# Kernel optimization log

Measured on AMD Instinct MI355X. Metric: run time of the kernel, lower is better.

Reference implementation:

```python
import jax, jax.numpy as jnp
import numpy as np

DIM = 512
MAXP = 100
N_SAMPLED = MAXP - 2  # partitions 0 (whole) and 1 (singletons) handled analytically
KMAX = 6              # sampled partitions have 2..6 parts


def _make_part_masks(dim, n_sampled, kmax, seed=0):
    rng = np.random.default_rng(seed)
    masks = np.zeros((n_sampled, kmax, dim), dtype=bool)
    for p in range(n_sampled):
        n_parts = rng.integers(2, kmax + 1)
        assign = rng.integers(0, n_parts, size=dim)
        for k in range(n_parts):
            masks[p, k] = assign == k
    return masks


def setup_inputs() -> dict:
    key = jax.random.key(0)
    ks = jax.random.split(key, 10)
    B, S, D = 8, 4096, DIM
    x = jax.random.normal(ks[0], (B, S, D), dtype=jnp.float32)
    entropy_scales = jnp.ones((D,), dtype=jnp.float32)
    integration_weights = jnp.ones((MAXP,), dtype=jnp.float32)
    W1 = jax.random.normal(ks[1], (32, 1), dtype=jnp.float32) * 0.5
    b1 = jax.random.normal(ks[2], (32,), dtype=jnp.float32) * 0.1
    W2 = jax.random.normal(ks[3], (16, 32), dtype=jnp.float32) * 0.2
    b2 = jax.random.normal(ks[4], (16,), dtype=jnp.float32) * 0.1
    W3 = jax.random.normal(ks[5], (1, 16), dtype=jnp.float32) * 0.3
    b3 = jax.random.normal(ks[6], (1,), dtype=jnp.float32) * 0.1
    part_masks = jnp.asarray(_make_part_masks(D, N_SAMPLED, KMAX))  # [P,K,D] bool
    return {"x": x, "entropy_scales": entropy_scales,
            "integration_weights": integration_weights,
            "W1": W1, "b1": b1, "W2": W2, "b2": b2, "W3": W3, "b3": b3,
            "part_masks": part_masks}


def _phi(x, entropy_scales, integration_weights, W1, b1, W2, b2, W3, b3, part_masks):
    B, S, D = x.shape
    # ---- full-flatten entropy (per batch), H(softmax(x.reshape(B,-1))) ----
    lp = jax.nn.log_softmax(x.reshape(B, -1), axis=-1)
    H_full = -jnp.sum(jnp.exp(lp) * lp, axis=-1)                     # [B]
    h_full_scaled = H_full * entropy_scales.mean()                   # [B]
    h_whole = H_full.mean()                                          # partition idx 0

    # ---- singleton partition (idx 1): softmax over seq per (b,d) ----
    lps = jax.nn.log_softmax(x, axis=1)                              # [B,S,D]
    H_sd = -jnp.sum(jnp.exp(lps) * lps, axis=1)                      # [B,D]
    h_single = H_sd.mean(axis=0).sum()

    # ---- sampled partitions via masks: per part, softmax over (seq x part dims) ----
    xmax_d = x.max(axis=1)                                           # [B,D]
    ex = jnp.exp(x - xmax_d[:, None, :])                             # [B,S,D]
    e_d = ex.sum(axis=1)                                             # [B,D] sum exp(x - xmax_d)
    t_d = (ex * x).sum(axis=1)                                       # [B,D] sum exp(.)*x
    valid = part_masks.any(axis=-1)                                  # [P,K]
    neg = jnp.finfo(x.dtype).min
    gmax = jnp.max(jnp.where(part_masks[None], xmax_d[:, None, None, :], neg), axis=-1)  # [B,P,K]
    gmax = jnp.where(valid[None], gmax, 0.0)
    shift = jnp.exp(xmax_d[:, None, None, :] - gmax[..., None])      # [B,P,K,D] <= 1
    mf = part_masks.astype(x.dtype)
    Z = jnp.einsum('pkd,bd,bpkd->bpk', mf, e_d, shift)               # group partition fn
    T = jnp.einsum('pkd,bd,bpkd->bpk', mf, t_d, shift)
    Zs = jnp.where(valid[None], Z, 1.0)
    H_pk = gmax + jnp.log(Zs) - T / Zs                               # group entropy [B,P,K]
    H_pk = jnp.where(valid[None], H_pk, 0.0)
    h_sampled = H_pk.mean(axis=0).sum(axis=-1)                       # [P] sum of part entropies

    h_parts = jnp.concatenate([jnp.stack([h_whole, h_single]), h_sampled])   # [100]
    weighted = h_parts * jax.nn.sigmoid(integration_weights[: h_parts.shape[0]])
    min_part = weighted.min()

    raw_phi = h_full_scaled.mean() - min_part
    z = jnp.clip(raw_phi / 10.0, 0.0, 1.0)[None]                     # [1]
    h = jax.nn.relu(z @ W1.T + b1)
    h = jax.nn.relu(h @ W2.T + b2)
    conf = jax.nn.sigmoid(h @ W3.T + b3).squeeze(-1)                 # scalar
    return conf


def reference(x, entropy_scales, integration_weights, W1, b1, W2, b2, W3, b3, part_masks):
    return _phi(x, entropy_scales, integration_weights, W1, b1, W2, b2, W3, b3, part_masks)
```

## Files before the change

kernel.cpp:

```cpp
#include <hip/hip_runtime.h>
#include <math.h>

constexpr int Bv = 8;
constexpr int Sv = 4096;
constexpr int Dv = 512;
constexpr int NCv = 64;
constexpr int SCv = Sv / NCv;
constexpr int Pv = 98;
constexpr int Kv = 6;
constexpr int MAXPv = 100;
constexpr int GPv = 14;
constexpr int PPGv = 7;

typedef float v4f __attribute__((ext_vector_type(4)));

constexpr size_t OFF_MPART = 0;
constexpr size_t OFF_ZPART = OFF_MPART + (size_t)Bv * NCv * Dv;
constexpr size_t OFF_TPART = OFF_ZPART + (size_t)Bv * NCv * Dv;
constexpr size_t OFF_HFULL = OFF_TPART + (size_t)Bv * NCv * Dv;
constexpr size_t OFF_HSD   = OFF_HFULL + Bv;
constexpr size_t OFF_HBP   = OFF_HSD + Bv;

__device__ __forceinline__ float warpSum(float v) {
    for (int o = 32; o > 0; o >>= 1) v += __shfl_xor(v, o);
    return v;
}
__device__ __forceinline__ float warpMax(float v) {
    for (int o = 32; o > 0; o >>= 1) v = fmaxf(v, __shfl_xor(v, o));
    return v;
}
__device__ __forceinline__ float blockSum512(float v, float* red) {
    float s = warpSum(v);
    int lane = threadIdx.x & 63, w = threadIdx.x >> 6;
    __syncthreads();
    if (lane == 0) red[w] = s;
    __syncthreads();
    return red[0] + red[1] + red[2] + red[3] + red[4] + red[5] + red[6] + red[7];
}
__device__ __forceinline__ float blockMax512(float v, float* red) {
    float s = warpMax(v);
    int lane = threadIdx.x & 63, w = threadIdx.x >> 6;
    __syncthreads();
    if (lane == 0) red[w] = s;
    __syncthreads();
    float m = red[0];
    for (int i = 1; i < 8; i++) m = fmaxf(m, red[i]);
    return m;
}

#define UPD(v, m, z, t)                                        \
    {                                                          \
        float vv = (v);                                        \
        if (vv > m) {                                          \
            float r = __expf(m - vv);                          \
            z = z * r + 1.0f;                                  \
            t = t * r + vv;                                    \
            m = vv;                                            \
        } else {                                               \
            float e_ = __expf(vv - m);                         \
            z += e_;                                           \
            t += e_ * vv;                                      \
        }                                                      \
    }

__device__ __forceinline__ void mergeStats(float& m, float& z, float& t,
                                           float mb, float zb, float tb) {
    float nm = fmaxf(m, mb);
    float ra = __expf(m - nm);
    float rb = __expf(mb - nm);
    z = z * ra + zb * rb;
    t = t * ra + tb * rb;
    m = nm;
}

__device__ __forceinline__ float sigmoidf(float v) { return 1.0f / (1.0f + __expf(-v)); }

__global__ __launch_bounds__(512) void k1_partial(const float* __restrict__ x,
                                                  float* __restrict__ ws) {
    int c = blockIdx.x;
    int b = blockIdx.y;
    int tid = threadIdx.x;
    int dg = tid & 127;
    int sl = tid >> 7;

    const v4f* xv = (const v4f*)x;
    float m0 = -INFINITY, m1 = -INFINITY, m2 = -INFINITY, m3 = -INFINITY;
    float z0 = 0.f, z1 = 0.f, z2 = 0.f, z3 = 0.f;
    float t0 = 0.f, t1 = 0.f, t2 = 0.f, t3 = 0.f;

    int sbase = c * SCv + sl;
#pragma unroll 4
    for (int i = 0; i < SCv / 4; i++) {
        int s = sbase + 4 * i;
        v4f v = __builtin_nontemporal_load(&xv[((size_t)b * Sv + s) * 128 + dg]);
        UPD(v.x, m0, z0, t0);
        UPD(v.y, m1, z1, t1);
        UPD(v.z, m2, z2, t2);
        UPD(v.w, m3, z3, t3);
    }

    __shared__ float smm[1024], smz[1024], smt[1024];
    if (sl == 1 || sl == 3) {
        int base = (sl >> 1) * 512 + dg * 4;
        smm[base + 0] = m0; smm[base + 1] = m1; smm[base + 2] = m2; smm[base + 3] = m3;
        smz[base + 0] = z0; smz[base + 1] = z1; smz[base + 2] = z2; smz[base + 3] = z3;
        smt[base + 0] = t0; smt[base + 1] = t1; smt[base + 2] = t2; smt[base + 3] = t3;
    }
    __syncthreads();
    if (sl == 0 || sl == 2) {
        int base = (sl >> 1) * 512 + dg * 4;
        mergeStats(m0, z0, t0, smm[base + 0], smz[base + 0], smt[base + 0]);
        mergeStats(m1, z1, t1, smm[base + 1], smz[base + 1], smt[base + 1]);
        mergeStats(m2, z2, t2, smm[base + 2], smz[base + 2], smt[base + 2]);
        mergeStats(m3, z3, t3, smm[base + 3], smz[base + 3], smt[base + 3]);
    }
    __syncthreads();
    if (sl == 2) {
        int base = dg * 4;
        smm[base + 0] = m0; smm[base + 1] = m1; smm[base + 2] = m2; smm[base + 3] = m3;
        smz[base + 0] = z0; smz[base + 1] = z1; smz[base + 2] = z2; smz[base + 3] = z3;
        smt[base + 0] = t0; smt[base + 1] = t1; smt[base + 2] = t2; smt[base + 3] = t3;
    }
    __syncthreads();
    if (sl == 0) {
        int base = dg * 4;
        mergeStats(m0, z0, t0, smm[base + 0], smz[base + 0], smt[base + 0]);
        mergeStats(m1, z1, t1, smm[base + 1], smz[base + 1], smt[base + 1]);
        mergeStats(m2, z2, t2, smm[base + 2], smz[base + 2], smt[base + 2]);
        mergeStats(m3, z3, t3, smm[base + 3], smz[base + 3], smt[base + 3]);

        size_t o = ((size_t)(b * NCv + c)) * 128 + dg;
        ((v4f*)(ws + OFF_MPART))[o] = (v4f){m0, m1, m2, m3};
        ((v4f*)(ws + OFF_ZPART))[o] = (v4f){z0, z1, z2, z3};
        ((v4f*)(ws + OFF_TPART))[o] = (v4f){t0, t1, t2, t3};
    }
}

__global__ __launch_bounds__(512) void k23_parts(const void* __restrict__ masks,
                                                 float* __restrict__ ws) {
    int g = blockIdx.x;
    int b = blockIdx.y;
    int d = threadIdx.x;
    int lane = d & 63, w = d >> 6;

    const float* mp = ws + OFF_MPART;
    const float* zp = ws + OFF_ZPART;
    const float* tp = ws + OFF_TPART;

    float ma = -INFINITY, za = 0.f, ta = 0.f;
    float mb2 = -INFINITY, zb2 = 0.f, tb2 = 0.f;
    for (int c = 0; c < NCv / 2; c++) {
        size_t ia = ((size_t)(b * NCv + c)) * Dv + d;
        size_t ib = ((size_t)(b * NCv + c + NCv / 2)) * Dv + d;
        mergeStats(ma, za, ta, mp[ia], zp[ia], tp[ia]);
        mergeStats(mb2, zb2, tb2, mp[ib], zp[ib], tp[ib]);
    }
    mergeStats(ma, za, ta, mb2, zb2, tb2);
    float xm = ma, e = za, t = ta;

    __shared__ float red[8];
    if (g == 0) {
        float hsd = xm + __logf(e) - t / e;
        float sum_h = blockSum512(hsd, red);
        float mbk = blockMax512(xm, red);
        float sc = __expf(xm - mbk);
        float zb = blockSum512(e * sc, red);
        float tb = blockSum512(t * sc, red);
        if (d == 0) {
            ws[OFF_HSD + b] = sum_h;
            ws[OFF_HFULL + b] = mbk + __logf(zb) - tb / zb;
        }
    }

    __shared__ int f;
    if (d == 0) f = 0;
    __syncthreads();
    if (((const unsigned int*)masks)[d] > 1u) f = 1;
    __syncthreads();
    int is_u8 = f;

    __shared__ float lmax[8 * Kv], lz[8 * Kv], lt[8 * Kv];
    __shared__ float gmax[Kv], hk[Kv];

    for (int i = 0; i < PPGv; i++) {
        int p = g * PPGv + i;

        int mk = 255;
        if (is_u8) {
            const unsigned char* mbyt = (const unsigned char*)masks;
            for (int k = 0; k < Kv; k++)
                if (mbyt[((size_t)p * Kv + k) * Dv + d]) { mk = k; break; }
        } else {
            const int* mint = (const int*)masks;
            for (int k = 0; k < Kv; k++)
                if (mint[((size_t)p * Kv + k) * Dv + d]) { mk = k; break; }
        }

        for (int k = 0; k < Kv; k++) {
            float cv = (mk == k) ? xm : -INFINITY;
            float wm = warpMax(cv);
            if (lane == 0) lmax[w * Kv + k] = wm;
        }
        __syncthreads();
        if (d < Kv) {
            float gm = lmax[d];
            for (int ww = 1; ww < 8; ww++) gm = fmaxf(gm, lmax[ww * Kv + d]);
            gmax[d] = gm;
        }
        __syncthreads();

        int mks = (mk < Kv) ? mk : 0;
        float gm = gmax[mks];
        float s = __expf(xm - gm);
        float ez = e * s, tz = t * s;
        for (int k = 0; k < Kv; k++) {
            float cz = (mk == k) ? ez : 0.f;
            float ctv = (mk == k) ? tz : 0.f;
            float sz = warpSum(cz);
            float st = warpSum(ctv);
            if (lane == 0) { lz[w * Kv + k] = sz; lt[w * Kv + k] = st; }
        }
        __syncthreads();
        if (d < Kv) {
            float Z = 0.f, T = 0.f;
            for (int ww = 0; ww < 8; ww++) { Z += lz[ww * Kv + d]; T += lt[ww * Kv + d]; }
            float gmv = gmax[d];
            hk[d] = (gmv > -INFINITY) ? gmv + __logf(Z) - T / Z : 0.f;
        }
        __syncthreads();
        if (d == 0)
            ws[OFF_HBP + (size_t)b * Pv + p] =
                hk[0] + hk[1] + hk[2] + hk[3] + hk[4] + hk[5];
        __syncthreads();
    }
}

__global__ __launch_bounds__(128) void k4_final(
    const float* __restrict__ es, const float* __restrict__ iw,
    const float* __restrict__ W1, const float* __restrict__ b1,
    const float* __restrict__ W2, const float* __restrict__ b2,
    const float* __restrict__ W3, const float* __restrict__ b3,
    const float* __restrict__ ws, float* __restrict__ out) {
    int tid = threadIdx.x;
    __shared__ float wgt[MAXPv];
    __shared__ float meanH_s;
    __shared__ float red[2];

    float v = es[tid] + es[tid + 128] + es[tid + 256] + es[tid + 384];
    float s64 = warpSum(v);
    int lane = tid & 63, w = tid >> 6;
    if (lane == 0) red[w] = s64;
    __syncthreads();
    float es_mean = (red[0] + red[1]) * (1.0f / 512.0f);

    if (tid < Pv) {
        float s = 0.f;
        for (int b = 0; b < Bv; b++) s += ws[OFF_HBP + (size_t)b * Pv + tid];
        wgt[tid + 2] = (s * (1.0f / Bv)) * sigmoidf(iw[tid + 2]);
    } else if (tid == Pv) {
        float s = 0.f;
        for (int b = 0; b < Bv; b++) s += ws[OFF_HFULL + b];
        float mh = s * (1.0f / Bv);
        meanH_s = mh;
        wgt[0] = mh * sigmoidf(iw[0]);
    } else if (tid == Pv + 1) {
        float s = 0.f;
        for (int b = 0; b < Bv; b++) s += ws[OFF_HSD + b];
        wgt[1] = (s * (1.0f / Bv)) * sigmoidf(iw[1]);
    }
    __syncthreads();

    if (tid == 0) {
        float mn = wgt[0];
        for (int i = 1; i < MAXPv; i++) mn = fminf(mn, wgt[i]);
        float raw = es_mean * meanH_s - mn;
        float z = fminf(fmaxf(raw * 0.1f, 0.0f), 1.0f);

        float h1[32];
        for (int j = 0; j < 32; j++) {
            float a = z * W1[j] + b1[j];
            h1[j] = a > 0.f ? a : 0.f;
        }
        float h2[16];
        for (int i = 0; i < 16; i++) {
            float a = b2[i];
            for (int j = 0; j < 32; j++) a += W2[i * 32 + j] * h1[j];
            h2[i] = a > 0.f ? a : 0.f;
        }
        float a = b3[0];
        for (int i = 0; i < 16; i++) a += W3[i] * h2[i];
        out[0] = sigmoidf(a);
    }
}

extern "C" void kernel_launch(void* const* d_in, const int* in_sizes, int n_in,
                              void* d_out, int out_size, void* d_ws, size_t ws_size,
                              hipStream_t stream) {
    const float* x  = (const float*)d_in[0];
    const float* es = (const float*)d_in[1];
    const float* iw = (const float*)d_in[2];
    const float* W1 = (const float*)d_in[3];
    const float* b1 = (const float*)d_in[4];
    const float* W2 = (const float*)d_in[5];
    const float* b2 = (const float*)d_in[6];
    const float* W3 = (const float*)d_in[7];
    const float* b3 = (const float*)d_in[8];
    const void* masks = d_in[9];
    float* ws = (float*)d_ws;
    float* out = (float*)d_out;

    k1_partial<<<dim3(NCv, Bv), dim3(512), 0, stream>>>(x, ws);
    k23_parts<<<dim3(GPv, Bv), dim3(512), 0, stream>>>(masks, ws);
    k4_final<<<dim3(1), dim3(128), 0, stream>>>(es, iw, W1, b1, W2, b2, W3, b3, ws, out);
}
```

Baseline: 166.8 us.

## Split chunk combine into separate kernel and parallelize partitions one per block

The chunk-statistics merge that each of the 14×8 partition blocks redundantly recomputed is moved into a dedicated per-batch combine kernel. That kernel writes the per-(b,d) max, partition function and T to the workspace and also computes the full and singleton entropies. The partition kernel then runs one block per (partition, batch), 98×8 blocks, loading the precombined stats instead of looping over 7 partitions serially. This removes redundant reads of the partial stats and raises parallelism, at the cost of an extra kernel launch.

Result: faster. 152.2 us (-8.8%).

```diff
diff --git a/kernel.cpp b/kernel.cpp
--- a/kernel.cpp
+++ b/kernel.cpp
@@ -9,15 +9,16 @@
 constexpr int Pv = 98;
 constexpr int Kv = 6;
 constexpr int MAXPv = 100;
-constexpr int GPv = 14;
-constexpr int PPGv = 7;
 
 typedef float v4f __attribute__((ext_vector_type(4)));
 
 constexpr size_t OFF_MPART = 0;
 constexpr size_t OFF_ZPART = OFF_MPART + (size_t)Bv * NCv * Dv;
 constexpr size_t OFF_TPART = OFF_ZPART + (size_t)Bv * NCv * Dv;
-constexpr size_t OFF_HFULL = OFF_TPART + (size_t)Bv * NCv * Dv;
+constexpr size_t OFF_XMAX  = OFF_TPART + (size_t)Bv * NCv * Dv;
+constexpr size_t OFF_ED    = OFF_XMAX + (size_t)Bv * Dv;
+constexpr size_t OFF_TD    = OFF_ED   + (size_t)Bv * Dv;
+constexpr size_t OFF_HFULL = OFF_TD   + (size_t)Bv * Dv;
 constexpr size_t OFF_HSD   = OFF_HFULL + Bv;
 constexpr size_t OFF_HBP   = OFF_HSD + Bv;
 
@@ -136,103 +137,158 @@
     }
 }
 
-__global__ __launch_bounds__(512) void k23_parts(const void* __restrict__ masks,
-                                                 float* __restrict__ ws) {
-    int g = blockIdx.x;
+__global__ __launch_bounds__(512) void k2_combine(float* __restrict__ ws) {
+    int b = blockIdx.x;
+    int tid = threadIdx.x;
+    int dg = tid & 127;
+    int ci = tid >> 7;
+
+    const v4f* mp = (const v4f*)(ws + OFF_MPART);
+    const v4f* zp = (const v4f*)(ws + OFF_ZPART);
+    const v4f* tp = (const v4f*)(ws + OFF_TPART);
+
+    float m0 = -INFINITY, m1 = -INFINITY, m2 = -INFINITY, m3 = -INFINITY;
+    float z0 = 0.f, z1 = 0.f, z2 = 0.f, z3 = 0.f;
+    float t0 = 0.f, t1 = 0.f, t2 = 0.f, t3 = 0.f;
+
+#pragma unroll 4
+    for (int i = 0; i < NCv / 4; i++) {
+        int c = ci + 4 * i;
+        size_t o = ((size_t)(b * NCv + c)) * 128 + dg;
+        v4f vm = mp[o], vz = zp[o], vt = tp[o];
+        mergeStats(m0, z0, t0, vm.x, vz.x, vt.x);
+        mergeStats(m1, z1, t1, vm.y, vz.y, vt.y);
+        mergeStats(m2, z2, t2, vm.z, vz.z, vt.z);
+        mergeStats(m3, z3, t3, vm.w, vz.w, vt.w);
+    }
+
+    __shared__ float smm[1024], smz[1024], smt[1024];
+    __shared__ float red[8];
+    if (ci == 1 || ci == 3) {
+        int base = (ci >> 1) * 512 + dg * 4;
+        smm[base + 0] = m0; smm[base + 1] = m1; smm[base + 2] = m2; smm[base + 3] = m3;
+        smz[base + 0] = z0; smz[base + 1] = z1; smz[base + 2] = z2; smz[base + 3] = z3;
+        smt[base + 0] = t0; smt[base + 1] = t1; smt[base + 2] = t2; smt[base + 3] = t3;
+    }
+    __syncthreads();
+    if (ci == 0 || ci == 2) {
+        int base = (ci >> 1) * 512 + dg * 4;
+        mergeStats(m0, z0, t0, smm[base + 0], smz[base + 0], smt[base + 0]);
+        mergeStats(m1, z1, t1, smm[base + 1], smz[base + 1], smt[base + 1]);
+        mergeStats(m2, z2, t2, smm[base + 2], smz[base + 2], smt[base + 2]);
+        mergeStats(m3, z3, t3, smm[base + 3], smz[base + 3], smt[base + 3]);
+    }
+    __syncthreads();
+    if (ci == 2) {
+        int base = dg * 4;
+        smm[base + 0] = m0; smm[base + 1] = m1; smm[base + 2] = m2; smm[base + 3] = m3;
+        smz[base + 0] = z0; smz[base + 1] = z1; smz[base + 2] = z2; smz[base + 3] = z3;
+        smt[base + 0] = t0; smt[base + 1] = t1; smt[base + 2] = t2; smt[base + 3] = t3;
+    }
+    __syncthreads();
+
+    float hsd_part = 0.f;
+    float mloc = -INFINITY;
+    if (ci == 0) {
+        int base = dg * 4;
+        mergeStats(m0, z0, t0, smm[base + 0], smz[base + 0], smt[base + 0]);
+        mergeStats(m1, z1, t1, smm[base + 1], smz[base + 1], smt[base + 1]);
+        mergeStats(m2, z2, t2, smm[base + 2], smz[base + 2], smt[base + 2]);
+        mergeStats(m3, z3, t3, smm[base + 3], smz[base + 3], smt[base + 3]);
+
+        size_t o = (size_t)b * 128 + dg;
+        ((v4f*)(ws + OFF_XMAX))[o] = (v4f){m0, m1, m2, m3};
+        ((v4f*)(ws + OFF_ED))[o]   = (v4f){z0, z1, z2, z3};
+        ((v4f*)(ws + OFF_TD))[o]   = (v4f){t0, t1, t2, t3};
+
+        hsd_part = (m0 + __logf(z0) - t0 / z0) + (m1 + __logf(z1) - t1 / z1) +
+                   (m2 + __logf(z2) - t2 / z2) + (m3 + __logf(z3) - t3 / z3);
+        mloc = fmaxf(fmaxf(m0, m1), fmaxf(m2, m3));
+    }
+
+    float sum_h = blockSum512(hsd_part, red);
+    float mb = blockMax512(mloc, red);
+    float zc = 0.f, tc = 0.f;
+    if (ci == 0) {
+        float s0 = __expf(m0 - mb), s1 = __expf(m1 - mb);
+        float s2 = __expf(m2 - mb), s3 = __expf(m3 - mb);
+        zc = z0 * s0 + z1 * s1 + z2 * s2 + z3 * s3;
+        tc = t0 * s0 + t1 * s1 + t2 * s2 + t3 * s3;
+    }
+    float zb = blockSum512(zc, red);
+    float tb = blockSum512(tc, red);
+    if (tid == 0) {
+        ws[OFF_HSD + b] = sum_h;
+        ws[OFF_HFULL + b] = mb + __logf(zb) - tb / zb;
+    }
+}
+
+__global__ __launch_bounds__(512) void k3_parts(const void* __restrict__ masks,
+                                                float* __restrict__ ws) {
+    int p = blockIdx.x;
     int b = blockIdx.y;
     int d = threadIdx.x;
     int lane = d & 63, w = d >> 6;
 
-    const float* mp = ws + OFF_MPART;
-    const float* zp = ws + OFF_ZPART;
-    const float* tp = ws + OFF_TPART;
-
-    float ma = -INFINITY, za = 0.f, ta = 0.f;
-    float mb2 = -INFINITY, zb2 = 0.f, tb2 = 0.f;
-    for (int c = 0; c < NCv / 2; c++) {
-        size_t ia = ((size_t)(b * NCv + c)) * Dv + d;
-        size_t ib = ((size_t)(b * NCv + c + NCv / 2)) * Dv + d;
-        mergeStats(ma, za, ta, mp[ia], zp[ia], tp[ia]);
-        mergeStats(mb2, zb2, tb2, mp[ib], zp[ib], tp[ib]);
-    }
-    mergeStats(ma, za, ta, mb2, zb2, tb2);
-    float xm = ma, e = za, t = ta;
-
-    __shared__ float red[8];
-    if (g == 0) {
-        float hsd = xm + __logf(e) - t / e;
-        float sum_h = blockSum512(hsd, red);
-        float mbk = blockMax512(xm, red);
-        float sc = __expf(xm - mbk);
-        float zb = blockSum512(e * sc, red);
-        float tb = blockSum512(t * sc, red);
-        if (d == 0) {
-            ws[OFF_HSD + b] = sum_h;
-            ws[OFF_HFULL + b] = mbk + __logf(zb) - tb / zb;
-        }
-    }
-
     __shared__ int f;
     if (d == 0) f = 0;
     __syncthreads();
     if (((const unsigned int*)masks)[d] > 1u) f = 1;
     __syncthreads();
-    int is_u8 = f;
+
+    int mk = 255;
+    if (f) {
+        const unsigned char* mbyt = (const unsigned char*)masks;
+        for (int k = 0; k < Kv; k++)
+            if (mbyt[((size_t)p * Kv + k) * Dv + d]) { mk = k; break; }
+    } else {
+        const int* mint = (const int*)masks;
+        for (int k = 0; k < Kv; k++)
+            if (mint[((size_t)p * Kv + k) * Dv + d]) { mk = k; break; }
+    }
+
+    float xm = ws[OFF_XMAX + (size_t)b * Dv + d];
+    float e  = ws[OFF_ED   + (size_t)b * Dv + d];
+    float t  = ws[OFF_TD   + (size_t)b * Dv + d];
 
     __shared__ float lmax[8 * Kv], lz[8 * Kv], lt[8 * Kv];
     __shared__ float gmax[Kv], hk[Kv];
 
-    for (int i = 0; i < PPGv; i++) {
-        int p = g * PPGv + i;
-
-        int mk = 255;
-        if (is_u8) {
-            const unsigned char* mbyt = (const unsigned char*)masks;
-            for (int k = 0; k < Kv; k++)
-                if (mbyt[((size_t)p * Kv + k) * Dv + d]) { mk = k; break; }
-        } else {
-            const int* mint = (const int*)masks;
-            for (int k = 0; k < Kv; k++)
-                if (mint[((size_t)p * Kv + k) * Dv + d]) { mk = k; break; }
-        }
-
-        for (int k = 0; k < Kv; k++) {
-            float cv = (mk == k) ? xm : -INFINITY;
-            float wm = warpMax(cv);
-            if (lane == 0) lmax[w * Kv + k] = wm;
-        }
-        __syncthreads();
-        if (d < Kv) {
-            float gm = lmax[d];
-            for (int ww = 1; ww < 8; ww++) gm = fmaxf(gm, lmax[ww * Kv + d]);
-            gmax[d] = gm;
-        }
-        __syncthreads();
-
-        int mks = (mk < Kv) ? mk : 0;
-        float gm = gmax[mks];
-        float s = __expf(xm - gm);
-        float ez = e * s, tz = t * s;
-        for (int k = 0; k < Kv; k++) {
-            float cz = (mk == k) ? ez : 0.f;
-            float ctv = (mk == k) ? tz : 0.f;
-            float sz = warpSum(cz);
-            float st = warpSum(ctv);
-            if (lane == 0) { lz[w * Kv + k] = sz; lt[w * Kv + k] = st; }
-        }
-        __syncthreads();
-        if (d < Kv) {
-            float Z = 0.f, T = 0.f;
-            for (int ww = 0; ww < 8; ww++) { Z += lz[ww * Kv + d]; T += lt[ww * Kv + d]; }
-            float gmv = gmax[d];
-            hk[d] = (gmv > -INFINITY) ? gmv + __logf(Z) - T / Z : 0.f;
-        }
-        __syncthreads();
-        if (d == 0)
-            ws[OFF_HBP + (size_t)b * Pv + p] =
-                hk[0] + hk[1] + hk[2] + hk[3] + hk[4] + hk[5];
-        __syncthreads();
-    }
+    for (int k = 0; k < Kv; k++) {
+        float cv = (mk == k) ? xm : -INFINITY;
+        float wm = warpMax(cv);
+        if (lane == 0) lmax[w * Kv + k] = wm;
+    }
+    __syncthreads();
+    if (d < Kv) {
+        float gm = lmax[d];
+        for (int ww = 1; ww < 8; ww++) gm = fmaxf(gm, lmax[ww * Kv + d]);
+        gmax[d] = gm;
+    }
+    __syncthreads();
+
+    int mks = (mk < Kv) ? mk : 0;
+    float gm = gmax[mks];
+    float s = __expf(xm - gm);
+    float ez = e * s, tz = t * s;
+    for (int k = 0; k < Kv; k++) {
+        float cz = (mk == k) ? ez : 0.f;
+        float ctv = (mk == k) ? tz : 0.f;
+        float sz = warpSum(cz);
+        float st = warpSum(ctv);
+        if (lane == 0) { lz[w * Kv + k] = sz; lt[w * Kv + k] = st; }
+    }
+    __syncthreads();
+    if (d < Kv) {
+        float Z = 0.f, T = 0.f;
+        for (int ww = 0; ww < 8; ww++) { Z += lz[ww * Kv + d]; T += lt[ww * Kv + d]; }
+        float gmv = gmax[d];
+        hk[d] = (gmv > -INFINITY) ? gmv + __logf(Z) - T / Z : 0.f;
+    }
+    __syncthreads();
+    if (d == 0)
+        ws[OFF_HBP + (size_t)b * Pv + p] =
+            hk[0] + hk[1] + hk[2] + hk[3] + hk[4] + hk[5];
 }
 
 __global__ __launch_bounds__(128) void k4_final(
@@ -310,6 +366,7 @@
     float* out = (float*)d_out;
 
     k1_partial<<<dim3(NCv, Bv), dim3(512), 0, stream>>>(x, ws);
-    k23_parts<<<dim3(GPv, Bv), dim3(512), 0, stream>>>(masks, ws);
+    k2_combine<<<dim3(Bv), dim3(512), 0, stream>>>(ws);
+    k3_parts<<<dim3(Pv, Bv), dim3(512), 0, stream>>>(masks, ws);
     k4_final<<<dim3(1), dim3(128), 0, stream>>>(es, iw, W1, b1, W2, b2, W3, b3, ws, out);
 }
```
